# Kernel tuning notes

Measured on AMD Instinct MI355X. Metric: run time of the kernel, lower is better.

Reference implementation:

```python
import jax, jax.numpy as jnp
import numpy as np

N = 100000   # nodes
E = 1600000  # edges (avg degree 16)
DIN, DH, DOUT = 128, 64, 40


def setup_inputs() -> dict:
    key = jax.random.key(0)
    ks = jax.random.split(key, 6)
    x = jax.random.normal(ks[0], (N, DIN), dtype=jnp.float32)
    edge_index = jax.random.randint(ks[1], (2, E), 0, N, dtype=jnp.int32)
    s1 = float(1.0 / np.sqrt(DIN))
    s2 = float(1.0 / np.sqrt(DH))
    W1 = jax.random.uniform(ks[2], (DIN, DH), jnp.float32, -s1, s1)
    b1 = jax.random.uniform(ks[3], (DH,), jnp.float32, -s1, s1)
    W2 = jax.random.uniform(ks[4], (DH, DOUT), jnp.float32, -s2, s2)
    b2 = jax.random.uniform(ks[5], (DOUT,), jnp.float32, -s2, s2)
    return {"x": x, "W1": W1, "b1": b1, "W2": W2, "b2": b2, "edge_index": edge_index}


def _gcn_conv(x, W, b, src, dst):
    """PyG GCNConv: add self-loops, symmetric degree normalization, scatter-add."""
    n = x.shape[0]
    h = x @ W  # [N, F_out] — transform before propagation (PyG order)
    ones = jnp.ones(src.shape[0], dtype=h.dtype)
    deg = jax.ops.segment_sum(ones, dst, num_segments=n) + 1.0  # +1 for self-loop
    dinv = jax.lax.rsqrt(deg)  # deg >= 1, no zero guard needed
    norm = dinv[src] * dinv[dst]  # [E]
    agg = jax.ops.segment_sum(h[src] * norm[:, None], dst, num_segments=n)
    agg = agg + h * (dinv * dinv)[:, None]  # self-loop messages
    return agg + b


def reference(x, W1, b1, W2, b2, edge_index):
    src, dst = edge_index[0], edge_index[1]
    h = jax.nn.relu(_gcn_conv(x, W1, b1, src, dst))
    out = _gcn_conv(h, W2, b2, src, dst)
    return jax.nn.log_softmax(out, axis=1)
```

## Files before the change

kernel.cpp:

```cpp
#include <hip/hip_runtime.h>
#include <hip/hip_fp16.h>
#include <math.h>

#define N_NODES 100000
#define N_EDGES 1600000
#define DIN 128
#define DH 64
#define DOUT 40

#define NB 256
#define BN 391
#define CAP 8192
#define BIN_BLOCKS 256
#define EPB 6250

typedef unsigned short u16;
typedef unsigned int u32;

__device__ inline __half2 u2h(u32 u) {
    union { u32 x; __half2 h; } c; c.x = u; return c.h;
}
__device__ inline u32 h2u(__half2 h) {
    union { __half2 h; u32 x; } c; c.h = h; return c.x;
}


__global__ __launch_bounds__(1024) void k_bin(const int* __restrict__ src,
                                              const int* __restrict__ dst,
                                              int* __restrict__ gcur,
                                              u32* __restrict__ staged) {
    __shared__ int hist[NB];
    __shared__ int base[NB];
    __shared__ int cur[NB];
    int t = threadIdx.x;
    for (int i = t; i < NB; i += 1024) { hist[i] = 0; cur[i] = 0; }
    __syncthreads();
    int e0 = blockIdx.x * EPB;
    int e1 = e0 + EPB; if (e1 > N_EDGES) e1 = N_EDGES;
    for (int e = e0 + t; e < e1; e += 1024)
        atomicAdd(&hist[dst[e] / BN], 1);
    __syncthreads();
    for (int i = t; i < NB; i += 1024) {
        int h = hist[i];
        base[i] = h ? atomicAdd(&gcur[i], h) : 0;
    }
    __syncthreads();
    for (int e = e0 + t; e < e1; e += 1024) {
        int d = dst[e], s = src[e];
        int b = d / BN;
        int dl = d - b * BN;
        int r = base[b] + atomicAdd(&cur[b], 1);
        if (r < CAP) staged[(size_t)b * CAP + r] = (u32)s | ((u32)dl << 17);
    }
}


__global__ __launch_bounds__(256) void k_csr(const int* __restrict__ gcur,
                                             const u32* __restrict__ staged,
                                             int* __restrict__ csr,
                                             int4* __restrict__ meta,
                                             float* __restrict__ dinv) {
    __shared__ u32 sedge[CAP];
    __shared__ int lcsr[CAP];
    __shared__ int hist[BN];
    __shared__ int lrs[BN];
    __shared__ int cur[BN];
    __shared__ int sbuf[256];
    int b = blockIdx.x, t = threadIdx.x;

    int part = 0;
    for (int i = t; i < b; i += 256) {
        int c = gcur[i]; if (c > CAP) c = CAP;
        part += c;
    }
    sbuf[t] = part;
    __syncthreads();
    for (int off = 128; off; off >>= 1) {
        if (t < off) sbuf[t] += sbuf[t + off];
        __syncthreads();
    }
    int base_ = sbuf[0];
    __syncthreads();

    int cnt = gcur[b]; if (cnt > CAP) cnt = CAP;
    for (int i = t; i < BN; i += 256) hist[i] = 0;
    for (int i = t; i < cnt; i += 256) sedge[i] = staged[(size_t)b * CAP + i];
    __syncthreads();
    for (int i = t; i < cnt; i += 256) atomicAdd(&hist[sedge[i] >> 17], 1);
    __syncthreads();

    int v0 = (2 * t < BN) ? hist[2 * t] : 0;
    int v1 = (2 * t + 1 < BN) ? hist[2 * t + 1] : 0;
    int s = v0 + v1;
    sbuf[t] = s;
    __syncthreads();
    for (int off = 1; off < 256; off <<= 1) {
        int add = (t >= off) ? sbuf[t - off] : 0;
        __syncthreads();
        sbuf[t] += add;
        __syncthreads();
    }
    int excl = sbuf[t] - s;
    if (2 * t < BN)     { lrs[2 * t] = excl;      cur[2 * t] = excl; }
    if (2 * t + 1 < BN) { lrs[2 * t + 1] = excl + v0; cur[2 * t + 1] = excl + v0; }
    __syncthreads();

    for (int i = t; i < cnt; i += 256) {
        u32 p = sedge[i];
        int pos = atomicAdd(&cur[p >> 17], 1);
        lcsr[pos] = (int)((p & 0x1FFFF) << 3);
    }
    __syncthreads();

    for (int i = t; i < cnt; i += 256) csr[base_ + i] = lcsr[i];
    int n0 = b * BN;
    for (int i = t; i < BN; i += 256) {
        int n = n0 + i;
        if (n < N_NODES) {
            int dg = hist[i];
            float dv = rsqrtf((float)dg + 1.0f);
            meta[n] = make_int4(base_ + lrs[i], dg, __float_as_int(dv), 0);
            dinv[n] = dv;
        }
    }
}


__global__ __launch_bounds__(256) void k_gemm1(const float* __restrict__ x,
                                               const float* __restrict__ W1,
                                               const float* __restrict__ dinv,
                                               u16* __restrict__ h1s) {
    __shared__ float xs[64 * 140];
    __shared__ float wsh[DIN * DH];
    int t = threadIdx.x;
    int row0 = blockIdx.x * 64;

    for (int it = 0; it < 8; ++it) {
        int idx = (it * 256 + t) * 4;
        int r = idx >> 7, c = idx & 127;
        float4 v = make_float4(0.f, 0.f, 0.f, 0.f);
        if (row0 + r < N_NODES) v = *(const float4*)&x[(size_t)(row0 + r) * DIN + c];
        *(float4*)&xs[r * 140 + c] = v;
    }
    for (int it = 0; it < 8; ++it) {
        int idx = (it * 256 + t) * 4;
        *(float4*)&wsh[idx] = *(const float4*)&W1[idx];
    }
    __syncthreads();

    int tr = t & 15;
    int tc = t >> 4;
    float acc[4][4] = {};
    for (int kb = 0; kb < DIN; kb += 4) {
        float4 w0 = *(const float4*)&wsh[(kb + 0) * DH + tr * 4];
        float4 w1 = *(const float4*)&wsh[(kb + 1) * DH + tr * 4];
        float4 w2 = *(const float4*)&wsh[(kb + 2) * DH + tr * 4];
        float4 w3 = *(const float4*)&wsh[(kb + 3) * DH + tr * 4];
#pragma unroll
        for (int i = 0; i < 4; ++i) {
            float4 xv = *(const float4*)&xs[(tc * 4 + i) * 140 + kb];
            acc[i][0] += xv.x * w0.x; acc[i][1] += xv.x * w0.y;
            acc[i][2] += xv.x * w0.z; acc[i][3] += xv.x * w0.w;
            acc[i][0] += xv.y * w1.x; acc[i][1] += xv.y * w1.y;
            acc[i][2] += xv.y * w1.z; acc[i][3] += xv.y * w1.w;
            acc[i][0] += xv.z * w2.x; acc[i][1] += xv.z * w2.y;
            acc[i][2] += xv.z * w2.z; acc[i][3] += xv.z * w2.w;
            acc[i][0] += xv.w * w3.x; acc[i][1] += xv.w * w3.y;
            acc[i][2] += xv.w * w3.z; acc[i][3] += xv.w * w3.w;
        }
    }
#pragma unroll
    for (int i = 0; i < 4; ++i) {
        int row = row0 + tc * 4 + i;
        if (row < N_NODES) {
            float dv = dinv[row];
            ushort4 o;
            o.x = __half_as_ushort(__float2half(acc[i][0] * dv));
            o.y = __half_as_ushort(__float2half(acc[i][1] * dv));
            o.z = __half_as_ushort(__float2half(acc[i][2] * dv));
            o.w = __half_as_ushort(__float2half(acc[i][3] * dv));
            *(ushort4*)&h1s[(size_t)row * DH + tr * 4] = o;
        }
    }
}


__global__ __launch_bounds__(256) void k_agg1(const u16* __restrict__ h1s,
                                              const int4* __restrict__ meta,
                                              const int* __restrict__ csr,
                                              const float* __restrict__ b1,
                                              float* __restrict__ h1) {
    int node = blockIdx.x * 4 + (threadIdx.x >> 6);
    if (node >= N_NODES) return;
    node = __builtin_amdgcn_readfirstlane(node);
    int lane = threadIdx.x & 63;
    int es = lane >> 3, fq = lane & 7;
    int4 me = meta[node];
    int s0 = me.x, d = me.y;
    float dv = __int_as_float(me.z);
    const uint4* rows = (const uint4*)h1s;
    __half2 A0 = __float2half2_rn(0.f), A1 = A0, A2 = A0, A3 = A0;
    if (es == 0) {
        uint4 v = rows[(u32)(node * 8 + fq)];
        A0 = u2h(v.x); A1 = u2h(v.y); A2 = u2h(v.z); A3 = u2h(v.w);
    }
    for (int base = 0; base < d; base += 64) {
        int nn = d - base; if (nn > 64) nn = 64;
        int myidx = (lane < nn) ? csr[s0 + base + lane] : 0;
        int j = 0;
        for (; j + 16 <= nn; j += 16) {
            int x0 = __builtin_amdgcn_ds_bpermute((j + es) * 4, myidx);
            int x1 = __builtin_amdgcn_ds_bpermute((j + 8 + es) * 4, myidx);
            uint4 v0 = rows[(u32)(x0 + fq)];
            uint4 v1 = rows[(u32)(x1 + fq)];
            A0 = __hadd2(A0, u2h(v0.x)); A1 = __hadd2(A1, u2h(v0.y));
            A2 = __hadd2(A2, u2h(v0.z)); A3 = __hadd2(A3, u2h(v0.w));
            A0 = __hadd2(A0, u2h(v1.x)); A1 = __hadd2(A1, u2h(v1.y));
            A2 = __hadd2(A2, u2h(v1.z)); A3 = __hadd2(A3, u2h(v1.w));
        }
        for (; j < nn; j += 8) {
            int x = __builtin_amdgcn_ds_bpermute((j + es) * 4, myidx);
            if (j + es < nn) {
                uint4 v = rows[(u32)(x + fq)];
                A0 = __hadd2(A0, u2h(v.x)); A1 = __hadd2(A1, u2h(v.y));
                A2 = __hadd2(A2, u2h(v.z)); A3 = __hadd2(A3, u2h(v.w));
            }
        }
    }
#pragma unroll
    for (int off = 8; off <= 32; off <<= 1) {
        A0 = __hadd2(A0, u2h((u32)__shfl_xor((int)h2u(A0), off, 64)));
        A1 = __hadd2(A1, u2h((u32)__shfl_xor((int)h2u(A1), off, 64)));
        A2 = __hadd2(A2, u2h((u32)__shfl_xor((int)h2u(A2), off, 64)));
        A3 = __hadd2(A3, u2h((u32)__shfl_xor((int)h2u(A3), off, 64)));
    }
    if (es == 0) {
        float4 bva = ((const float4*)b1)[fq * 2 + 0];
        float4 bvb = ((const float4*)b1)[fq * 2 + 1];
        float4 oa, ob;
        oa.x = fmaxf(__low2float(A0)  * dv + bva.x, 0.f);
        oa.y = fmaxf(__high2float(A0) * dv + bva.y, 0.f);
        oa.z = fmaxf(__low2float(A1)  * dv + bva.z, 0.f);
        oa.w = fmaxf(__high2float(A1) * dv + bva.w, 0.f);
        ob.x = fmaxf(__low2float(A2)  * dv + bvb.x, 0.f);
        ob.y = fmaxf(__high2float(A2) * dv + bvb.y, 0.f);
        ob.z = fmaxf(__low2float(A3)  * dv + bvb.z, 0.f);
        ob.w = fmaxf(__high2float(A3) * dv + bvb.w, 0.f);
        ((float4*)h1)[(u32)(node * 16 + fq * 2 + 0)] = oa;
        ((float4*)h1)[(u32)(node * 16 + fq * 2 + 1)] = ob;
    }
}


__global__ __launch_bounds__(256) void k_gemm2(const float* __restrict__ h1,
                                               const float* __restrict__ W2,
                                               const float* __restrict__ dinv,
                                               u16* __restrict__ h2s) {
    __shared__ float xs[64 * 68];
    __shared__ float wsh[DH * DOUT];
    int t = threadIdx.x;
    int row0 = blockIdx.x * 64;

    for (int it = 0; it < 4; ++it) {
        int idx = (it * 256 + t) * 4;
        int r = idx >> 6, c = idx & 63;
        float4 v = make_float4(0.f, 0.f, 0.f, 0.f);
        if (row0 + r < N_NODES) v = *(const float4*)&h1[(size_t)(row0 + r) * DH + c];
        *(float4*)&xs[r * 68 + c] = v;
    }
    for (int idx = t * 4; idx < DH * DOUT; idx += 1024) {
        *(float4*)&wsh[idx] = *(const float4*)&W2[idx];
    }
    __syncthreads();

    int fg = t & 7;
    int rg = t >> 3;
    float acc[2][5] = {};
    for (int k = 0; k < DH; ++k) {
        float x0 = xs[(rg * 2 + 0) * 68 + k];
        float x1 = xs[(rg * 2 + 1) * 68 + k];
#pragma unroll
        for (int j = 0; j < 5; ++j) {
            float w = wsh[k * DOUT + fg * 5 + j];
            acc[0][j] += x0 * w;
            acc[1][j] += x1 * w;
        }
    }
#pragma unroll
    for (int i = 0; i < 2; ++i) {
        int row = row0 + rg * 2 + i;
        if (row < N_NODES) {
            float dvv = dinv[row];
#pragma unroll
            for (int j = 0; j < 5; ++j)
                h2s[(size_t)row * 64 + fg * 5 + j] =
                    __half_as_ushort(__float2half(acc[i][j] * dvv));
        }
    }
}


__global__ __launch_bounds__(256) void k_agg2(const u16* __restrict__ h2s,
                                              const int4* __restrict__ meta,
                                              const int* __restrict__ csr,
                                              const float* __restrict__ b2,
                                              float* __restrict__ out) {
    int node = blockIdx.x * 4 + (threadIdx.x >> 6);
    if (node >= N_NODES) return;
    node = __builtin_amdgcn_readfirstlane(node);
    int lane = threadIdx.x & 63;
    int es = lane >> 3, fq = lane & 7;
    bool act = fq < 5;
    int4 me = meta[node];
    int s0 = me.x, d = me.y;
    float dv = __int_as_float(me.z);
    const uint4* rows = (const uint4*)h2s;
    __half2 A0 = __float2half2_rn(0.f), A1 = A0, A2 = A0, A3 = A0;
    if (es == 0 && act) {
        uint4 v = rows[(u32)(node * 8 + fq)];
        A0 = u2h(v.x); A1 = u2h(v.y); A2 = u2h(v.z); A3 = u2h(v.w);
    }
    for (int base = 0; base < d; base += 64) {
        int nn = d - base; if (nn > 64) nn = 64;
        int myidx = (lane < nn) ? csr[s0 + base + lane] : 0;
        int j = 0;
        for (; j + 16 <= nn; j += 16) {
            int x0 = __builtin_amdgcn_ds_bpermute((j + es) * 4, myidx);
            int x1 = __builtin_amdgcn_ds_bpermute((j + 8 + es) * 4, myidx);
            if (act) {
                uint4 v0 = rows[(u32)(x0 + fq)];
                uint4 v1 = rows[(u32)(x1 + fq)];
                A0 = __hadd2(A0, u2h(v0.x)); A1 = __hadd2(A1, u2h(v0.y));
                A2 = __hadd2(A2, u2h(v0.z)); A3 = __hadd2(A3, u2h(v0.w));
                A0 = __hadd2(A0, u2h(v1.x)); A1 = __hadd2(A1, u2h(v1.y));
                A2 = __hadd2(A2, u2h(v1.z)); A3 = __hadd2(A3, u2h(v1.w));
            }
        }
        for (; j < nn; j += 8) {
            int x = __builtin_amdgcn_ds_bpermute((j + es) * 4, myidx);
            if (act && j + es < nn) {
                uint4 v = rows[(u32)(x + fq)];
                A0 = __hadd2(A0, u2h(v.x)); A1 = __hadd2(A1, u2h(v.y));
                A2 = __hadd2(A2, u2h(v.z)); A3 = __hadd2(A3, u2h(v.w));
            }
        }
    }
#pragma unroll
    for (int off = 8; off <= 32; off <<= 1) {
        A0 = __hadd2(A0, u2h((u32)__shfl_xor((int)h2u(A0), off, 64)));
        A1 = __hadd2(A1, u2h((u32)__shfl_xor((int)h2u(A1), off, 64)));
        A2 = __hadd2(A2, u2h((u32)__shfl_xor((int)h2u(A2), off, 64)));
        A3 = __hadd2(A3, u2h((u32)__shfl_xor((int)h2u(A3), off, 64)));
    }

    float4 bva = act ? ((const float4*)b2)[fq * 2 + 0] : make_float4(0.f, 0.f, 0.f, 0.f);
    float4 bvb = act ? ((const float4*)b2)[fq * 2 + 1] : make_float4(0.f, 0.f, 0.f, 0.f);
    float v0 = act ? __low2float(A0)  * dv + bva.x : -INFINITY;
    float v1 = act ? __high2float(A0) * dv + bva.y : -INFINITY;
    float v2 = act ? __low2float(A1)  * dv + bva.z : -INFINITY;
    float v3 = act ? __high2float(A1) * dv + bva.w : -INFINITY;
    float v4 = act ? __low2float(A2)  * dv + bvb.x : -INFINITY;
    float v5 = act ? __high2float(A2) * dv + bvb.y : -INFINITY;
    float v6 = act ? __low2float(A3)  * dv + bvb.z : -INFINITY;
    float v7 = act ? __high2float(A3) * dv + bvb.w : -INFINITY;
    float m = fmaxf(fmaxf(fmaxf(v0, v1), fmaxf(v2, v3)),
                    fmaxf(fmaxf(v4, v5), fmaxf(v6, v7)));
    m = fmaxf(m, __shfl_xor(m, 1, 64));
    m = fmaxf(m, __shfl_xor(m, 2, 64));
    m = fmaxf(m, __shfl_xor(m, 4, 64));
    float ex = 0.f;
    if (act) {
        ex = __expf(v0 - m) + __expf(v1 - m) + __expf(v2 - m) + __expf(v3 - m)
           + __expf(v4 - m) + __expf(v5 - m) + __expf(v6 - m) + __expf(v7 - m);
    }
    ex += __shfl_xor(ex, 1, 64);
    ex += __shfl_xor(ex, 2, 64);
    ex += __shfl_xor(ex, 4, 64);
    float lse = m + __logf(ex);
    if (es == 0 && act) {
        float4 oa = make_float4(v0 - lse, v1 - lse, v2 - lse, v3 - lse);
        float4 ob = make_float4(v4 - lse, v5 - lse, v6 - lse, v7 - lse);
        *(float4*)&out[(u32)(node * 40 + fq * 8 + 0)] = oa;
        *(float4*)&out[(u32)(node * 40 + fq * 8 + 4)] = ob;
    }
}


extern "C" void kernel_launch(void* const* d_in, const int* in_sizes, int n_in,
                              void* d_out, int out_size, void* d_ws, size_t ws_size,
                              hipStream_t stream) {
    const float* x  = (const float*)d_in[0];
    const float* W1 = (const float*)d_in[1];
    const float* b1 = (const float*)d_in[2];
    const float* W2 = (const float*)d_in[3];
    const float* b2 = (const float*)d_in[4];
    const int* eidx = (const int*)d_in[5];
    const int* srcp = eidx;
    const int* dstp = eidx + N_EDGES;
    float* out = (float*)d_out;

    char* w = (char*)d_ws;
    int* gcur    = (int*)w;   w += sizeof(int) * NB;
    float* dinv  = (float*)w; w += sizeof(float) * N_NODES + 48;
    int4* meta   = (int4*)w;  w += sizeof(int4) * N_NODES;
    u32* staged  = (u32*)w;   w += sizeof(u32) * (size_t)NB * CAP;
    int* csr     = (int*)w;   w += sizeof(int) * N_EDGES;
    u16* h1s     = (u16*)w;   w += sizeof(u16) * (size_t)N_NODES * DH;
    float* h1    = (float*)w; w += sizeof(float) * (size_t)N_NODES * DH;
    u16* h2s     = h1s;

    hipMemsetAsync(gcur, 0, sizeof(int) * NB, stream);
    k_bin<<<BIN_BLOCKS, 1024, 0, stream>>>(srcp, dstp, gcur, staged);
    k_csr<<<NB, 256, 0, stream>>>(gcur, staged, csr, meta, dinv);
    k_gemm1<<<(N_NODES + 63) / 64, 256, 0, stream>>>(x, W1, dinv, h1s);
    k_agg1<<<(N_NODES + 3) / 4, 256, 0, stream>>>(h1s, meta, csr, b1, h1);
    k_gemm2<<<(N_NODES + 63) / 64, 256, 0, stream>>>(h1, W2, dinv, h2s);
    k_agg2<<<(N_NODES + 3) / 4, 256, 0, stream>>>(h2s, meta, csr, b2, out);
}
```

Measured before the change: 203.0 us.

## Store layer-1 activations in fp16 and pack layer-2 rows to 40 halves

The aggregated hidden activations are now written as fp16 instead of fp32, halving the write in agg1 and the read in gemm2. The layer-2 transformed features are packed at a row stride of 40 halves instead of 64, so agg2 gathers 80-byte rows instead of 128-byte rows and touches fewer cache lines per edge. To support the variable stride, CSR entries now hold raw node ids and the gather kernels multiply by the row size. This adds an fp16 rounding step on the hidden layer and leaves 80-byte rows that are not aligned to cache lines.

```diff
diff --git a/kernel.cpp b/kernel.cpp
--- a/kernel.cpp
+++ b/kernel.cpp
@@ -108,7 +108,7 @@
     for (int i = t; i < cnt; i += 256) {
         u32 p = sedge[i];
         int pos = atomicAdd(&cur[p >> 17], 1);
-        lcsr[pos] = (int)((p & 0x1FFFF) << 3);
+        lcsr[pos] = (int)(p & 0x1FFFF);
     }
     __syncthreads();
 
@@ -189,7 +189,7 @@
                                               const int4* __restrict__ meta,
                                               const int* __restrict__ csr,
                                               const float* __restrict__ b1,
-                                              float* __restrict__ h1) {
+                                              u16* __restrict__ h1f) {
     int node = blockIdx.x * 4 + (threadIdx.x >> 6);
     if (node >= N_NODES) return;
     node = __builtin_amdgcn_readfirstlane(node);
@@ -211,8 +211,8 @@
         for (; j + 16 <= nn; j += 16) {
             int x0 = __builtin_amdgcn_ds_bpermute((j + es) * 4, myidx);
             int x1 = __builtin_amdgcn_ds_bpermute((j + 8 + es) * 4, myidx);
-            uint4 v0 = rows[(u32)(x0 + fq)];
-            uint4 v1 = rows[(u32)(x1 + fq)];
+            uint4 v0 = rows[(u32)(x0 * 8 + fq)];
+            uint4 v1 = rows[(u32)(x1 * 8 + fq)];
             A0 = __hadd2(A0, u2h(v0.x)); A1 = __hadd2(A1, u2h(v0.y));
             A2 = __hadd2(A2, u2h(v0.z)); A3 = __hadd2(A3, u2h(v0.w));
             A0 = __hadd2(A0, u2h(v1.x)); A1 = __hadd2(A1, u2h(v1.y));
@@ -221,7 +221,7 @@
         for (; j < nn; j += 8) {
             int x = __builtin_amdgcn_ds_bpermute((j + es) * 4, myidx);
             if (j + es < nn) {
-                uint4 v = rows[(u32)(x + fq)];
+                uint4 v = rows[(u32)(x * 8 + fq)];
                 A0 = __hadd2(A0, u2h(v.x)); A1 = __hadd2(A1, u2h(v.y));
                 A2 = __hadd2(A2, u2h(v.z)); A3 = __hadd2(A3, u2h(v.w));
             }
@@ -237,22 +237,25 @@
     if (es == 0) {
         float4 bva = ((const float4*)b1)[fq * 2 + 0];
         float4 bvb = ((const float4*)b1)[fq * 2 + 1];
-        float4 oa, ob;
-        oa.x = fmaxf(__low2float(A0)  * dv + bva.x, 0.f);
-        oa.y = fmaxf(__high2float(A0) * dv + bva.y, 0.f);
-        oa.z = fmaxf(__low2float(A1)  * dv + bva.z, 0.f);
-        oa.w = fmaxf(__high2float(A1) * dv + bva.w, 0.f);
-        ob.x = fmaxf(__low2float(A2)  * dv + bvb.x, 0.f);
-        ob.y = fmaxf(__high2float(A2) * dv + bvb.y, 0.f);
-        ob.z = fmaxf(__low2float(A3)  * dv + bvb.z, 0.f);
-        ob.w = fmaxf(__high2float(A3) * dv + bvb.w, 0.f);
-        ((float4*)h1)[(u32)(node * 16 + fq * 2 + 0)] = oa;
-        ((float4*)h1)[(u32)(node * 16 + fq * 2 + 1)] = ob;
-    }
-}
-
-
-__global__ __launch_bounds__(256) void k_gemm2(const float* __restrict__ h1,
+        float f0 = fmaxf(__low2float(A0)  * dv + bva.x, 0.f);
+        float f1 = fmaxf(__high2float(A0) * dv + bva.y, 0.f);
+        float f2 = fmaxf(__low2float(A1)  * dv + bva.z, 0.f);
+        float f3 = fmaxf(__high2float(A1) * dv + bva.w, 0.f);
+        float f4 = fmaxf(__low2float(A2)  * dv + bvb.x, 0.f);
+        float f5 = fmaxf(__high2float(A2) * dv + bvb.y, 0.f);
+        float f6 = fmaxf(__low2float(A3)  * dv + bvb.z, 0.f);
+        float f7 = fmaxf(__high2float(A3) * dv + bvb.w, 0.f);
+        uint4 ov;
+        ov.x = h2u(__floats2half2_rn(f0, f1));
+        ov.y = h2u(__floats2half2_rn(f2, f3));
+        ov.z = h2u(__floats2half2_rn(f4, f5));
+        ov.w = h2u(__floats2half2_rn(f6, f7));
+        ((uint4*)h1f)[(u32)(node * 8 + fq)] = ov;
+    }
+}
+
+
+__global__ __launch_bounds__(256) void k_gemm2(const u16* __restrict__ h1f,
                                                const float* __restrict__ W2,
                                                const float* __restrict__ dinv,
                                                u16* __restrict__ h2s) {
@@ -265,7 +268,12 @@
         int idx = (it * 256 + t) * 4;
         int r = idx >> 6, c = idx & 63;
         float4 v = make_float4(0.f, 0.f, 0.f, 0.f);
-        if (row0 + r < N_NODES) v = *(const float4*)&h1[(size_t)(row0 + r) * DH + c];
+        if (row0 + r < N_NODES) {
+            uint2 hv = *(const uint2*)&h1f[(size_t)(row0 + r) * DH + c];
+            __half2 hlo = u2h(hv.x), hhi = u2h(hv.y);
+            v = make_float4(__low2float(hlo), __high2float(hlo),
+                            __low2float(hhi), __high2float(hhi));
+        }
         *(float4*)&xs[r * 68 + c] = v;
     }
     for (int idx = t * 4; idx < DH * DOUT; idx += 1024) {
@@ -293,7 +301,7 @@
             float dvv = dinv[row];
 #pragma unroll
             for (int j = 0; j < 5; ++j)
-                h2s[(size_t)row * 64 + fg * 5 + j] =
+                h2s[(size_t)row * DOUT + fg * 5 + j] =
                     __half_as_ushort(__float2half(acc[i][j] * dvv));
         }
     }
@@ -317,7 +325,7 @@
     const uint4* rows = (const uint4*)h2s;
     __half2 A0 = __float2half2_rn(0.f), A1 = A0, A2 = A0, A3 = A0;
     if (es == 0 && act) {
-        uint4 v = rows[(u32)(node * 8 + fq)];
+        uint4 v = rows[(u32)(node * 5 + fq)];
         A0 = u2h(v.x); A1 = u2h(v.y); A2 = u2h(v.z); A3 = u2h(v.w);
     }
     for (int base = 0; base < d; base += 64) {
@@ -328,8 +336,8 @@
             int x0 = __builtin_amdgcn_ds_bpermute((j + es) * 4, myidx);
             int x1 = __builtin_amdgcn_ds_bpermute((j + 8 + es) * 4, myidx);
             if (act) {
-                uint4 v0 = rows[(u32)(x0 + fq)];
-                uint4 v1 = rows[(u32)(x1 + fq)];
+                uint4 v0 = rows[(u32)(x0 * 5 + fq)];
+                uint4 v1 = rows[(u32)(x1 * 5 + fq)];
                 A0 = __hadd2(A0, u2h(v0.x)); A1 = __hadd2(A1, u2h(v0.y));
                 A2 = __hadd2(A2, u2h(v0.z)); A3 = __hadd2(A3, u2h(v0.w));
                 A0 = __hadd2(A0, u2h(v1.x)); A1 = __hadd2(A1, u2h(v1.y));
@@ -339,7 +347,7 @@
         for (; j < nn; j += 8) {
             int x = __builtin_amdgcn_ds_bpermute((j + es) * 4, myidx);
             if (act && j + es < nn) {
-                uint4 v = rows[(u32)(x + fq)];
+                uint4 v = rows[(u32)(x * 5 + fq)];
                 A0 = __hadd2(A0, u2h(v.x)); A1 = __hadd2(A1, u2h(v.y));
                 A2 = __hadd2(A2, u2h(v.z)); A3 = __hadd2(A3, u2h(v.w));
             }
@@ -406,14 +414,14 @@
     u32* staged  = (u32*)w;   w += sizeof(u32) * (size_t)NB * CAP;
     int* csr     = (int*)w;   w += sizeof(int) * N_EDGES;
     u16* h1s     = (u16*)w;   w += sizeof(u16) * (size_t)N_NODES * DH;
-    float* h1    = (float*)w; w += sizeof(float) * (size_t)N_NODES * DH;
+    u16* h1f     = (u16*)w;   w += sizeof(u16) * (size_t)N_NODES * DH;
     u16* h2s     = h1s;
 
     hipMemsetAsync(gcur, 0, sizeof(int) * NB, stream);
     k_bin<<<BIN_BLOCKS, 1024, 0, stream>>>(srcp, dstp, gcur, staged);
     k_csr<<<NB, 256, 0, stream>>>(gcur, staged, csr, meta, dinv);
     k_gemm1<<<(N_NODES + 63) / 64, 256, 0, stream>>>(x, W1, dinv, h1s);
-    k_agg1<<<(N_NODES + 3) / 4, 256, 0, stream>>>(h1s, meta, csr, b1, h1);
-    k_gemm2<<<(N_NODES + 63) / 64, 256, 0, stream>>>(h1, W2, dinv, h2s);
+    k_agg1<<<(N_NODES + 3) / 4, 256, 0, stream>>>(h1s, meta, csr, b1, h1f);
+    k_gemm2<<<(N_NODES + 63) / 64, 256, 0, stream>>>(h1f, W2, dinv, h2s);
     k_agg2<<<(N_NODES + 3) / 4, 256, 0, stream>>>(h2s, meta, csr, b2, out);
 }
```

After: 202.2 us (median of 2 runs). No clear change (-0.4%).
